# Kernel optimization log

Hardware: AMD Instinct MI355X
Metric: run time of the kernel (lower is better)

## Reference

```python
import jax, jax.numpy as jnp
import numpy as np

E, K, H, I, T = 32, 4, 1024, 1024, 1024
ALPHA, BETA = 1.702, 1.0  # swiglu_alpha, swiglu_beta from the module


def setup_inputs() -> dict:
    key = jax.random.key(0)
    k0, k1, k2, k3 = jax.random.split(key, 4)
    return {
        "hidden_states": jax.random.normal(k0, (T, H), jnp.float32),
        "gate_w": jax.random.normal(k1, (H, E), jnp.float32) * (H ** -0.5),
        "gate_b": jnp.zeros((E,), jnp.float32),
        # pair_wise_act=True: gate/up are interleaved along the last dim of w1's output
        "w1": jax.random.normal(k2, (E, H, 2 * I), jnp.float32) * (H ** -0.5),
        "b1": jnp.zeros((E, 2 * I), jnp.float32),
        "w2": jax.random.normal(k3, (E, I, H), jnp.float32) * (I ** -0.5),
        "b2": jnp.zeros((E, H), jnp.float32),
    }


def reference(hidden_states, gate_w, gate_b, w1, b1, w2, b2):
    # Router gate (ReplicatedLinear with bias)
    router_logits = hidden_states @ gate_w + gate_b            # [T, E]
    probs = jax.nn.softmax(router_logits, axis=-1)
    topk_w, topk_idx = jax.lax.top_k(probs, K)                 # [T, K]
    # renormalize (norm_topk_prob=True)
    topk_w = topk_w / jnp.sum(topk_w, axis=-1, keepdims=True)
    # combine weights per (expert, token): sum over slots where idx == e
    onehot = (topk_idx[None, :, :] == jnp.arange(E)[:, None, None])  # [E, T, K]
    combine_w = jnp.sum(onehot * topk_w[None, :, :], axis=-1)        # [E, T]
    # Expert MLPs (grouped GEMM expressed as dense-per-expert einsum)
    h = jnp.einsum('th,ehd->etd', hidden_states, w1) + b1[:, None, :]  # [E, T, 2I]
    gate = h[..., 0::2]   # interleaved pairwise gate
    up = h[..., 1::2]     # interleaved pairwise up
    act = (up + BETA) * gate * jax.nn.sigmoid(ALPHA * gate)           # [E, T, I]
    y = jnp.einsum('eti,eih->eth', act, w2) + b2[:, None, :]          # [E, T, H]
    # weighted combine across selected experts
    return jnp.einsum('eth,et->th', y, combine_w)                     # [T, H]
```

## Files before the change

kernel.cpp:

```cpp
#include <hip/hip_runtime.h>
#include <hip/hip_bf16.h>
#include <math.h>

#define E_ 32
#define K_ 4
#define H_ 1024
#define I_ 1024
#define T_ 1024
#define TWO_I 2048

typedef __attribute__((ext_vector_type(4))) float float4v;
typedef __attribute__((ext_vector_type(8))) short short8v;
typedef __attribute__((ext_vector_type(4))) short short4v;

__device__ __forceinline__ unsigned short f2bf(float f) {
    unsigned u = __float_as_uint(f);
    u = (u + 0x7FFFu + ((u >> 16) & 1u)) >> 16;
    return (unsigned short)u;
}
__device__ __forceinline__ short4v cvt4(float4v v) {
    union { unsigned u[2]; short4v s; } r;
    asm("v_cvt_pk_bf16_f32 %0, %1, %2" : "=v"(r.u[0]) : "v"(v[0]), "v"(v[1]));
    asm("v_cvt_pk_bf16_f32 %0, %1, %2" : "=v"(r.u[1]) : "v"(v[2]), "v"(v[3]));
    return r.s;
}
__device__ __forceinline__ int permpos(int k4) {
    return ((k4 >> 5) << 5) + (((k4 >> 2) & 3) << 3) + (((k4 >> 4) & 1) << 2);
}

__global__ __launch_bounds__(256) void zero_kernel(float* __restrict__ out,
                                                   int* __restrict__ counts) {
    int i = blockIdx.x * 256 + threadIdx.x;
    *(float4v*)(out + (size_t)i * 4) = (float4v){0.f, 0.f, 0.f, 0.f};
    if (blockIdx.x == 0 && threadIdx.x < E_) counts[threadIdx.x] = 0;
}

__global__ __launch_bounds__(256) void hs2bf_kernel(
    const float* __restrict__ hs, unsigned short* __restrict__ hsb) {
    int i = blockIdx.x * 256 + threadIdx.x;
    float4v v = *(const float4v*)(hs + (size_t)i * 4);
    *(short4v*)(hsb + (size_t)i * 4) = cvt4(v);
}

__global__ __launch_bounds__(256) void router_kernel(
    const float* __restrict__ hs, const float* __restrict__ gw,
    const float* __restrict__ gb, int* __restrict__ counts,
    int* __restrict__ token_list, float* __restrict__ weight_list) {
    int wv = threadIdx.x >> 6, lane = threadIdx.x & 63;
    int t = blockIdx.x * 4 + wv;
    int e = lane & 31;
    int half = lane >> 5;
    const float* hrow = hs + (size_t)t * H_;
    const float* gcol = gw + e;
    float a0 = 0.f, a1 = 0.f;
    int hb = half * 512;
#pragma unroll 4
    for (int h = 0; h < 512; h += 2) {
        a0 = fmaf(hrow[hb + h],     gcol[(size_t)(hb + h) * E_], a0);
        a1 = fmaf(hrow[hb + h + 1], gcol[(size_t)(hb + h + 1) * E_], a1);
    }
    float part = a0 + a1;
    part += __shfl_xor(part, 32);
    float cur = part + gb[e];

    int idx4[K_]; float val4[K_];
#pragma unroll
    for (int k = 0; k < K_; ++k) {
        float m = cur;
#pragma unroll
        for (int d = 1; d < 64; d <<= 1) m = fmaxf(m, __shfl_xor(m, d));
        unsigned long long b = __ballot(cur == m);
        int l = __ffsll(b) - 1;
        idx4[k] = l & 31; val4[k] = m;
        if (e == (l & 31)) cur = -INFINITY;
    }
    float mx = val4[0], s = 0.f, wv4[K_];
#pragma unroll
    for (int k = 0; k < K_; ++k) { wv4[k] = expf(val4[k] - mx); s += wv4[k]; }
    float inv = 1.f / s;
    if (lane < K_) {
        int ex = idx4[lane];
        int slot = atomicAdd(&counts[ex], 1);
        token_list[ex * T_ + slot] = t;
        weight_list[ex * T_ + slot] = wv4[lane] * inv;
    }
}

#define G_COMPUTE(BUF)                                                         \
    _Pragma("unroll")                                                          \
    for (int s = 0; s < 2; ++s) {                                              \
        short8v afr[4];                                                        \
        _Pragma("unroll")                                                      \
        for (int mi = 0; mi < 4; ++mi) {                                       \
            int row = wm * 64 + mi * 16 + l15;                                 \
            afr[mi] = *(const short8v*)&As[BUF][row * 64 + ((s * 32 + g * 8) ^ sw)]; \
        }                                                                      \
        short4v bl[2], bh[2];                                                  \
        _Pragma("unroll")                                                      \
        for (int ni = 0; ni < 2; ++ni) {                                       \
            unsigned ad = ((BUF) ? trb1 : trb0) + (unsigned)(ni * 2048 + s * 1024); \
            asm volatile("ds_read_b64_tr_b16 %0, %1" : "=v"(bl[ni]) : "v"(ad));     \
            asm volatile("ds_read_b64_tr_b16 %0, %1" : "=v"(bh[ni]) : "v"(ad + 512u)); \
        }                                                                      \
        asm volatile("s_waitcnt lgkmcnt(0)" ::: "memory");                     \
        __builtin_amdgcn_sched_barrier(0);                                     \
        _Pragma("unroll")                                                      \
        for (int ni = 0; ni < 2; ++ni) {                                       \
            short8v b;                                                         \
            b[0] = bl[ni][0]; b[1] = bl[ni][1]; b[2] = bl[ni][2]; b[3] = bl[ni][3]; \
            b[4] = bh[ni][0]; b[5] = bh[ni][1]; b[6] = bh[ni][2]; b[7] = bh[ni][3]; \
            _Pragma("unroll")                                                  \
            for (int mi = 0; mi < 4; ++mi)                                     \
                acc[mi][ni] = __builtin_amdgcn_mfma_f32_16x16x32_bf16(afr[mi], b, acc[mi][ni], 0, 0, 0); \
        }                                                                      \
    }

#define G_STEP(BUF, KN, BSTRIDE, ISLAST)                                       \
    {                                                                          \
        __syncthreads();                                                       \
        if (!(ISLAST)) {                                                       \
            _Pragma("unroll")                                                  \
            for (int i = 0; i < 4; ++i)                                        \
                ra[i] = aptr[i] ? *(const short8v*)(aptr[i] + (KN)) : z8;      \
            _Pragma("unroll")                                                  \
            for (int i = 0; i < 4; ++i)                                        \
                rb[i] = *(const float4v*)(bptrB + (size_t)(KN) * (BSTRIDE) + (size_t)(i * 16) * (BSTRIDE)); \
        }                                                                      \
        __builtin_amdgcn_sched_barrier(0);                                     \
        G_COMPUTE(BUF)                                                         \
        if (!(ISLAST)) {                                                       \
            _Pragma("unroll")                                                  \
            for (int i = 0; i < 4; ++i) {                                      \
                short8v v = ra[i];                                             \
                short4v lo, hi;                                                \
                lo[0] = v[0]; lo[1] = v[1]; lo[2] = v[2]; lo[3] = v[3];        \
                hi[0] = v[4]; hi[1] = v[5]; hi[2] = v[6]; hi[3] = v[7];        \
                *(short4v*)&As[(BUF) ^ 1][aw0[i]] = lo;                        \
                *(short4v*)&As[(BUF) ^ 1][aw1[i]] = hi;                        \
            }                                                                  \
            _Pragma("unroll")                                                  \
            for (int i = 0; i < 4; ++i) *(short4v*)&Bs[(BUF) ^ 1][bwidx[i]] = cvt4(rb[i]); \
        }                                                                      \
    }

__global__ __launch_bounds__(256, 3) void gemm1_kernel(
    const unsigned short* __restrict__ hsb, const float* __restrict__ w1,
    const float* __restrict__ b1, const int* __restrict__ counts,
    const int* __restrict__ token_list, unsigned short* __restrict__ actb) {
    int e = blockIdx.z;
    int cnt = counts[e];
    int m0 = blockIdx.y * 128;
    if (m0 >= cnt) return;
    int cb = blockIdx.x * 64;
    const float* w1e = w1 + (size_t)e * H_ * TWO_I;
    const int* tl = token_list + e * T_;

    __shared__ __align__(16) short As[2][128 * 64];
    __shared__ __align__(16) short Bs[2][64 * 64];

    int tid = threadIdx.x;
    int lane = tid & 63;
    int wid = tid >> 6;
    int wm = wid >> 1, wn = wid & 1;
    int g = lane >> 4;
    int l15 = lane & 15;
    int sw = (l15 & 7) << 3;
    unsigned trb0 = (unsigned)(size_t)(&Bs[0][0]) + (unsigned)(lane * 8) + (unsigned)(wn * 4096);
    unsigned trb1 = (unsigned)(size_t)(&Bs[1][0]) + (unsigned)(lane * 8) + (unsigned)(wn * 4096);

    int q = tid & 7;
    const unsigned short* aptr[4]; int aw0[4], aw1[4];
#pragma unroll
    for (int i = 0; i < 4; ++i) {
        int row = i * 32 + (tid >> 3);
        int gr = m0 + row;
        aptr[i] = (gr < cnt) ? hsb + (size_t)tl[gr] * H_ + q * 8 : nullptr;
        int swr = (row & 7) << 3;
        aw0[i] = row * 64 + (permpos(q * 8) ^ swr);
        aw1[i] = row * 64 + (permpos(q * 8 + 4) ^ swr);
    }
    int c4 = (tid & 15) << 2;
    const float* bptrB = w1e + (size_t)(tid >> 4) * TWO_I + cb + c4;
    int bwidx[4];
#pragma unroll
    for (int i = 0; i < 4; ++i) {
        int krow = i * 16 + (tid >> 4);
        bwidx[i] = ((c4 >> 4) * 16 + (krow >> 2)) * 64 + (krow & 3) * 16 + (c4 & 15);
    }

    float4v acc[4][2];
#pragma unroll
    for (int i = 0; i < 4; ++i)
#pragma unroll
        for (int j = 0; j < 2; ++j) acc[i][j] = (float4v){0.f, 0.f, 0.f, 0.f};

    short8v ra[4]; float4v rb[4];
    const short8v z8 = {0, 0, 0, 0, 0, 0, 0, 0};
#pragma unroll
    for (int i = 0; i < 4; ++i) ra[i] = aptr[i] ? *(const short8v*)(aptr[i]) : z8;
#pragma unroll
    for (int i = 0; i < 4; ++i) rb[i] = *(const float4v*)(bptrB + (size_t)(i * 16) * TWO_I);
#pragma unroll
    for (int i = 0; i < 4; ++i) {
        short8v v = ra[i];
        short4v lo, hi;
        lo[0] = v[0]; lo[1] = v[1]; lo[2] = v[2]; lo[3] = v[3];
        hi[0] = v[4]; hi[1] = v[5]; hi[2] = v[6]; hi[3] = v[7];
        *(short4v*)&As[0][aw0[i]] = lo;
        *(short4v*)&As[0][aw1[i]] = hi;
    }
#pragma unroll
    for (int i = 0; i < 4; ++i) *(short4v*)&Bs[0][bwidx[i]] = cvt4(rb[i]);

#pragma unroll 1
    for (int kk = 0; kk < H_; kk += 128) {
        G_STEP(0, kk + 64, TWO_I, false)
        G_STEP(1, kk + 128, TWO_I, (kk + 128) >= H_)
    }

    const float* b1e = b1 + (size_t)e * TWO_I;
#pragma unroll
    for (int mi = 0; mi < 4; ++mi) {
#pragma unroll
        for (int r = 0; r < 4; ++r) {
            int gm = m0 + wm * 64 + mi * 16 + g * 4 + r;
#pragma unroll
            for (int ni = 0; ni < 2; ++ni) {
                float v = acc[mi][ni][r];
                float o = __shfl_xor(v, 1);
                if (!(lane & 1) && gm < cnt) {
                    int wc = cb + wn * 32 + ni * 16 + l15;
                    float gate = v + b1e[wc];
                    float up   = o + b1e[wc + 1];
                    float sg = 1.f / (1.f + __expf(-1.702f * gate));
                    float av = (up + 1.f) * gate * sg;
                    actb[(size_t)(e * T_ + gm) * I_ + (wc >> 1)] = f2bf(av);
                }
            }
        }
    }
}

__global__ __launch_bounds__(256, 3) void gemm2_kernel(
    const unsigned short* __restrict__ actb, const float* __restrict__ w2,
    const float* __restrict__ b2, const int* __restrict__ counts,
    const int* __restrict__ token_list, const float* __restrict__ weight_list,
    float* __restrict__ out) {
    int e = blockIdx.z;
    int cnt = counts[e];
    int m0 = blockIdx.y * 128;
    if (m0 >= cnt) return;
    int h0 = (blockIdx.x >> 1) * 64;
    int kbase = (blockIdx.x & 1) * 512;
    const float* w2e = w2 + (size_t)e * I_ * H_;
    const int* tl = token_list + e * T_;

    __shared__ __align__(16) short As[2][128 * 64];
    __shared__ __align__(16) short Bs[2][64 * 64];

    int tid = threadIdx.x;
    int lane = tid & 63;
    int wid = tid >> 6;
    int wm = wid >> 1, wn = wid & 1;
    int g = lane >> 4;
    int l15 = lane & 15;
    int sw = (l15 & 7) << 3;
    unsigned trb0 = (unsigned)(size_t)(&Bs[0][0]) + (unsigned)(lane * 8) + (unsigned)(wn * 4096);
    unsigned trb1 = (unsigned)(size_t)(&Bs[1][0]) + (unsigned)(lane * 8) + (unsigned)(wn * 4096);

    int q = tid & 7;
    const unsigned short* aptr[4]; int aw0[4], aw1[4];
#pragma unroll
    for (int i = 0; i < 4; ++i) {
        int row = i * 32 + (tid >> 3);
        int gr = m0 + row;
        aptr[i] = (gr < cnt) ? actb + (size_t)(e * T_ + gr) * I_ + kbase + q * 8 : nullptr;
        int swr = (row & 7) << 3;
        aw0[i] = row * 64 + (permpos(q * 8) ^ swr);
        aw1[i] = row * 64 + (permpos(q * 8 + 4) ^ swr);
    }
    int c4 = (tid & 15) << 2;
    const float* bptrB = w2e + (size_t)(kbase + (tid >> 4)) * H_ + h0 + c4;
    int bwidx[4];
#pragma unroll
    for (int i = 0; i < 4; ++i) {
        int krow = i * 16 + (tid >> 4);
        bwidx[i] = ((c4 >> 4) * 16 + (krow >> 2)) * 64 + (krow & 3) * 16 + (c4 & 15);
    }

    float4v acc[4][2];
#pragma unroll
    for (int i = 0; i < 4; ++i)
#pragma unroll
        for (int j = 0; j < 2; ++j) acc[i][j] = (float4v){0.f, 0.f, 0.f, 0.f};

    short8v ra[4]; float4v rb[4];
    const short8v z8 = {0, 0, 0, 0, 0, 0, 0, 0};
#pragma unroll
    for (int i = 0; i < 4; ++i) ra[i] = aptr[i] ? *(const short8v*)(aptr[i]) : z8;
#pragma unroll
    for (int i = 0; i < 4; ++i) rb[i] = *(const float4v*)(bptrB + (size_t)(i * 16) * H_);
#pragma unroll
    for (int i = 0; i < 4; ++i) {
        short8v v = ra[i];
        short4v lo, hi;
        lo[0] = v[0]; lo[1] = v[1]; lo[2] = v[2]; lo[3] = v[3];
        hi[0] = v[4]; hi[1] = v[5]; hi[2] = v[6]; hi[3] = v[7];
        *(short4v*)&As[0][aw0[i]] = lo;
        *(short4v*)&As[0][aw1[i]] = hi;
    }
#pragma unroll
    for (int i = 0; i < 4; ++i) *(short4v*)&Bs[0][bwidx[i]] = cvt4(rb[i]);

#pragma unroll 1
    for (int kk = 0; kk < 512; kk += 128) {
        G_STEP(0, kk + 64, H_, false)
        G_STEP(1, kk + 128, H_, (kk + 128) >= 512)
    }

    const float* b2e = b2 + (size_t)e * H_;
    const float* wl = weight_list + e * T_;
    bool addbias = (kbase == 0);
#pragma unroll
    for (int mi = 0; mi < 4; ++mi) {
#pragma unroll
        for (int r = 0; r < 4; ++r) {
            int gm = m0 + wm * 64 + mi * 16 + g * 4 + r;
            if (gm < cnt) {
                int t = tl[gm];
                float wgt = wl[gm];
#pragma unroll
                for (int ni = 0; ni < 2; ++ni) {
                    int h = h0 + wn * 32 + ni * 16 + l15;
                    float v = acc[mi][ni][r];
                    if (addbias) v += b2e[h];
                    atomicAdd(&out[(size_t)t * H_ + h], v * wgt);
                }
            }
        }
    }
}

extern "C" void kernel_launch(void* const* d_in, const int* in_sizes, int n_in,
                              void* d_out, int out_size, void* d_ws, size_t ws_size,
                              hipStream_t stream) {
    const float* hs = (const float*)d_in[0];
    const float* gw = (const float*)d_in[1];
    const float* gb = (const float*)d_in[2];
    const float* w1 = (const float*)d_in[3];
    const float* b1 = (const float*)d_in[4];
    const float* w2 = (const float*)d_in[5];
    const float* b2 = (const float*)d_in[6];
    float* out = (float*)d_out;

    char* ws = (char*)d_ws;
    int*   counts      = (int*)ws;
    int*   token_list  = (int*)(ws + 4096);
    float* weight_list = (float*)(ws + 4096 + 131072);
    unsigned short* hsb  = (unsigned short*)(ws + (1 << 20));
    unsigned short* actb = (unsigned short*)(ws + (1 << 20) + (2 << 20));

    zero_kernel<<<(T_ * H_ / 4) / 256, 256, 0, stream>>>(out, counts);
    hs2bf_kernel<<<(T_ * H_ / 4) / 256, 256, 0, stream>>>(hs, hsb);
    router_kernel<<<T_ / 4, 256, 0, stream>>>(hs, gw, gb, counts, token_list, weight_list);
    gemm1_kernel<<<dim3(TWO_I / 64, T_ / 128, E_), 256, 0, stream>>>(
        hsb, w1, b1, counts, token_list, actb);
    gemm2_kernel<<<dim3((H_ / 64) * 2, T_ / 128, E_), 256, 0, stream>>>(
        actb, w2, b2, counts, token_list, weight_list, out);
}
```

Measured before the change: 201.6 us.

## Widen gemm1 N-tile to 128 and fuse zero/convert prep kernels

Result: slower. 217.6 us (+8.0%).

```diff
diff --git a/kernel.cpp b/kernel.cpp
--- a/kernel.cpp
+++ b/kernel.cpp
@@ -28,18 +28,14 @@
     return ((k4 >> 5) << 5) + (((k4 >> 2) & 3) << 3) + (((k4 >> 4) & 1) << 2);
 }
 
-__global__ __launch_bounds__(256) void zero_kernel(float* __restrict__ out,
-                                                   int* __restrict__ counts) {
-    int i = blockIdx.x * 256 + threadIdx.x;
-    *(float4v*)(out + (size_t)i * 4) = (float4v){0.f, 0.f, 0.f, 0.f};
-    if (blockIdx.x == 0 && threadIdx.x < E_) counts[threadIdx.x] = 0;
-}
-
-__global__ __launch_bounds__(256) void hs2bf_kernel(
-    const float* __restrict__ hs, unsigned short* __restrict__ hsb) {
+__global__ __launch_bounds__(256) void prep_kernel(
+    const float* __restrict__ hs, unsigned short* __restrict__ hsb,
+    float* __restrict__ out, int* __restrict__ counts) {
     int i = blockIdx.x * 256 + threadIdx.x;
     float4v v = *(const float4v*)(hs + (size_t)i * 4);
     *(short4v*)(hsb + (size_t)i * 4) = cvt4(v);
+    *(float4v*)(out + (size_t)i * 4) = (float4v){0.f, 0.f, 0.f, 0.f};
+    if (blockIdx.x == 0 && threadIdx.x < E_) counts[threadIdx.x] = 0;
 }
 
 __global__ __launch_bounds__(256) void router_kernel(
@@ -86,7 +82,7 @@
     }
 }
 
-#define G_COMPUTE(BUF)                                                         \
+#define G1_COMPUTE(BUF)                                                        \
     _Pragma("unroll")                                                          \
     for (int s = 0; s < 2; ++s) {                                              \
         short8v afr[4];                                                        \
@@ -95,9 +91,9 @@
             int row = wm * 64 + mi * 16 + l15;                                 \
             afr[mi] = *(const short8v*)&As[BUF][row * 64 + ((s * 32 + g * 8) ^ sw)]; \
         }                                                                      \
-        short4v bl[2], bh[2];                                                  \
-        _Pragma("unroll")                                                      \
-        for (int ni = 0; ni < 2; ++ni) {                                       \
+        short4v bl[4], bh[4];                                                  \
+        _Pragma("unroll")                                                      \
+        for (int ni = 0; ni < 4; ++ni) {                                       \
             unsigned ad = ((BUF) ? trb1 : trb0) + (unsigned)(ni * 2048 + s * 1024); \
             asm volatile("ds_read_b64_tr_b16 %0, %1" : "=v"(bl[ni]) : "v"(ad));     \
             asm volatile("ds_read_b64_tr_b16 %0, %1" : "=v"(bh[ni]) : "v"(ad + 512u)); \
@@ -105,7 +101,7 @@
         asm volatile("s_waitcnt lgkmcnt(0)" ::: "memory");                     \
         __builtin_amdgcn_sched_barrier(0);                                     \
         _Pragma("unroll")                                                      \
-        for (int ni = 0; ni < 2; ++ni) {                                       \
+        for (int ni = 0; ni < 4; ++ni) {                                       \
             short8v b;                                                         \
             b[0] = bl[ni][0]; b[1] = bl[ni][1]; b[2] = bl[ni][2]; b[3] = bl[ni][3]; \
             b[4] = bh[ni][0]; b[5] = bh[ni][1]; b[6] = bh[ni][2]; b[7] = bh[ni][3]; \
@@ -115,7 +111,7 @@
         }                                                                      \
     }
 
-#define G_STEP(BUF, KN, BSTRIDE, ISLAST)                                       \
+#define G1_STEP(BUF, KN, ISLAST)                                               \
     {                                                                          \
         __syncthreads();                                                       \
         if (!(ISLAST)) {                                                       \
@@ -123,11 +119,11 @@
             for (int i = 0; i < 4; ++i)                                        \
                 ra[i] = aptr[i] ? *(const short8v*)(aptr[i] + (KN)) : z8;      \
             _Pragma("unroll")                                                  \
-            for (int i = 0; i < 4; ++i)                                        \
-                rb[i] = *(const float4v*)(bptrB + (size_t)(KN) * (BSTRIDE) + (size_t)(i * 16) * (BSTRIDE)); \
+            for (int i = 0; i < 8; ++i)                                        \
+                rb[i] = *(const float4v*)(bptr[i] + (size_t)(KN) * TWO_I);     \
         }                                                                      \
         __builtin_amdgcn_sched_barrier(0);                                     \
-        G_COMPUTE(BUF)                                                         \
+        G1_COMPUTE(BUF)                                                        \
         if (!(ISLAST)) {                                                       \
             _Pragma("unroll")                                                  \
             for (int i = 0; i < 4; ++i) {                                      \
@@ -139,11 +135,11 @@
                 *(short4v*)&As[(BUF) ^ 1][aw1[i]] = hi;                        \
             }                                                                  \
             _Pragma("unroll")                                                  \
-            for (int i = 0; i < 4; ++i) *(short4v*)&Bs[(BUF) ^ 1][bwidx[i]] = cvt4(rb[i]); \
-        }                                                                      \
-    }
-
-__global__ __launch_bounds__(256, 3) void gemm1_kernel(
+            for (int i = 0; i < 8; ++i) *(short4v*)&Bs[(BUF) ^ 1][bwidx[i]] = cvt4(rb[i]); \
+        }                                                                      \
+    }
+
+__global__ __launch_bounds__(256, 2) void gemm1_kernel(
     const unsigned short* __restrict__ hsb, const float* __restrict__ w1,
     const float* __restrict__ b1, const int* __restrict__ counts,
     const int* __restrict__ token_list, unsigned short* __restrict__ actb) {
@@ -151,12 +147,12 @@
     int cnt = counts[e];
     int m0 = blockIdx.y * 128;
     if (m0 >= cnt) return;
-    int cb = blockIdx.x * 64;
+    int cb = blockIdx.x * 128;
     const float* w1e = w1 + (size_t)e * H_ * TWO_I;
     const int* tl = token_list + e * T_;
 
     __shared__ __align__(16) short As[2][128 * 64];
-    __shared__ __align__(16) short Bs[2][64 * 64];
+    __shared__ __align__(16) short Bs[2][8192];
 
     int tid = threadIdx.x;
     int lane = tid & 63;
@@ -165,8 +161,8 @@
     int g = lane >> 4;
     int l15 = lane & 15;
     int sw = (l15 & 7) << 3;
-    unsigned trb0 = (unsigned)(size_t)(&Bs[0][0]) + (unsigned)(lane * 8) + (unsigned)(wn * 4096);
-    unsigned trb1 = (unsigned)(size_t)(&Bs[1][0]) + (unsigned)(lane * 8) + (unsigned)(wn * 4096);
+    unsigned trb0 = (unsigned)(size_t)(&Bs[0][0]) + (unsigned)(lane * 8) + (unsigned)(wn * 8192);
+    unsigned trb1 = (unsigned)(size_t)(&Bs[1][0]) + (unsigned)(lane * 8) + (unsigned)(wn * 8192);
 
     int q = tid & 7;
     const unsigned short* aptr[4]; int aw0[4], aw1[4];
@@ -179,27 +175,28 @@
         aw0[i] = row * 64 + (permpos(q * 8) ^ swr);
         aw1[i] = row * 64 + (permpos(q * 8 + 4) ^ swr);
     }
-    int c4 = (tid & 15) << 2;
-    const float* bptrB = w1e + (size_t)(tid >> 4) * TWO_I + cb + c4;
-    int bwidx[4];
-#pragma unroll
-    for (int i = 0; i < 4; ++i) {
-        int krow = i * 16 + (tid >> 4);
-        bwidx[i] = ((c4 >> 4) * 16 + (krow >> 2)) * 64 + (krow & 3) * 16 + (c4 & 15);
-    }
-
-    float4v acc[4][2];
+    const float* bptr[8]; int bwidx[8];
+#pragma unroll
+    for (int i = 0; i < 8; ++i) {
+        int c = i * 256 + tid;
+        int krow = c >> 5;
+        int n4 = (c & 31) << 2;
+        bptr[i] = w1e + (size_t)krow * TWO_I + cb + n4;
+        bwidx[i] = ((n4 >> 4) * 16 + (krow >> 2)) * 64 + (krow & 3) * 16 + (n4 & 15);
+    }
+
+    float4v acc[4][4];
 #pragma unroll
     for (int i = 0; i < 4; ++i)
 #pragma unroll
-        for (int j = 0; j < 2; ++j) acc[i][j] = (float4v){0.f, 0.f, 0.f, 0.f};
-
-    short8v ra[4]; float4v rb[4];
+        for (int j = 0; j < 4; ++j) acc[i][j] = (float4v){0.f, 0.f, 0.f, 0.f};
+
+    short8v ra[4]; float4v rb[8];
     const short8v z8 = {0, 0, 0, 0, 0, 0, 0, 0};
 #pragma unroll
     for (int i = 0; i < 4; ++i) ra[i] = aptr[i] ? *(const short8v*)(aptr[i]) : z8;
 #pragma unroll
-    for (int i = 0; i < 4; ++i) rb[i] = *(const float4v*)(bptrB + (size_t)(i * 16) * TWO_I);
+    for (int i = 0; i < 8; ++i) rb[i] = *(const float4v*)(bptr[i]);
 #pragma unroll
     for (int i = 0; i < 4; ++i) {
         short8v v = ra[i];
@@ -210,12 +207,12 @@
         *(short4v*)&As[0][aw1[i]] = hi;
     }
 #pragma unroll
-    for (int i = 0; i < 4; ++i) *(short4v*)&Bs[0][bwidx[i]] = cvt4(rb[i]);
+    for (int i = 0; i < 8; ++i) *(short4v*)&Bs[0][bwidx[i]] = cvt4(rb[i]);
 
 #pragma unroll 1
     for (int kk = 0; kk < H_; kk += 128) {
-        G_STEP(0, kk + 64, TWO_I, false)
-        G_STEP(1, kk + 128, TWO_I, (kk + 128) >= H_)
+        G1_STEP(0, kk + 64, false)
+        G1_STEP(1, kk + 128, (kk + 128) >= H_)
     }
 
     const float* b1e = b1 + (size_t)e * TWO_I;
@@ -225,11 +222,11 @@
         for (int r = 0; r < 4; ++r) {
             int gm = m0 + wm * 64 + mi * 16 + g * 4 + r;
 #pragma unroll
-            for (int ni = 0; ni < 2; ++ni) {
+            for (int ni = 0; ni < 4; ++ni) {
                 float v = acc[mi][ni][r];
                 float o = __shfl_xor(v, 1);
                 if (!(lane & 1) && gm < cnt) {
-                    int wc = cb + wn * 32 + ni * 16 + l15;
+                    int wc = cb + wn * 64 + ni * 16 + l15;
                     float gate = v + b1e[wc];
                     float up   = o + b1e[wc + 1];
                     float sg = 1.f / (1.f + __expf(-1.702f * gate));
@@ -240,6 +237,63 @@
         }
     }
 }
+
+#define G2_COMPUTE(BUF)                                                        \
+    _Pragma("unroll")                                                          \
+    for (int s = 0; s < 2; ++s) {                                              \
+        short8v afr[4];                                                        \
+        _Pragma("unroll")                                                      \
+        for (int mi = 0; mi < 4; ++mi) {                                       \
+            int row = wm * 64 + mi * 16 + l15;                                 \
+            afr[mi] = *(const short8v*)&As[BUF][row * 64 + ((s * 32 + g * 8) ^ sw)]; \
+        }                                                                      \
+        short4v bl[2], bh[2];                                                  \
+        _Pragma("unroll")                                                      \
+        for (int ni = 0; ni < 2; ++ni) {                                       \
+            unsigned ad = ((BUF) ? trb1 : trb0) + (unsigned)(ni * 2048 + s * 1024); \
+            asm volatile("ds_read_b64_tr_b16 %0, %1" : "=v"(bl[ni]) : "v"(ad));     \
+            asm volatile("ds_read_b64_tr_b16 %0, %1" : "=v"(bh[ni]) : "v"(ad + 512u)); \
+        }                                                                      \
+        asm volatile("s_waitcnt lgkmcnt(0)" ::: "memory");                     \
+        __builtin_amdgcn_sched_barrier(0);                                     \
+        _Pragma("unroll")                                                      \
+        for (int ni = 0; ni < 2; ++ni) {                                       \
+            short8v b;                                                         \
+            b[0] = bl[ni][0]; b[1] = bl[ni][1]; b[2] = bl[ni][2]; b[3] = bl[ni][3]; \
+            b[4] = bh[ni][0]; b[5] = bh[ni][1]; b[6] = bh[ni][2]; b[7] = bh[ni][3]; \
+            _Pragma("unroll")                                                  \
+            for (int mi = 0; mi < 4; ++mi)                                     \
+                acc[mi][ni] = __builtin_amdgcn_mfma_f32_16x16x32_bf16(afr[mi], b, acc[mi][ni], 0, 0, 0); \
+        }                                                                      \
+    }
+
+#define G2_STEP(BUF, KN, ISLAST)                                               \
+    {                                                                          \
+        __syncthreads();                                                       \
+        if (!(ISLAST)) {                                                       \
+            _Pragma("unroll")                                                  \
+            for (int i = 0; i < 4; ++i)                                        \
+                ra[i] = aptr[i] ? *(const short8v*)(aptr[i] + (KN)) : z8;      \
+            _Pragma("unroll")                                                  \
+            for (int i = 0; i < 4; ++i)                                        \
+                rb[i] = *(const float4v*)(bptrB + (size_t)(KN) * H_ + (size_t)(i * 16) * H_); \
+        }                                                                      \
+        __builtin_amdgcn_sched_barrier(0);                                     \
+        G2_COMPUTE(BUF)                                                        \
+        if (!(ISLAST)) {                                                       \
+            _Pragma("unroll")                                                  \
+            for (int i = 0; i < 4; ++i) {                                      \
+                short8v v = ra[i];                                             \
+                short4v lo, hi;                                                \
+                lo[0] = v[0]; lo[1] = v[1]; lo[2] = v[2]; lo[3] = v[3];        \
+                hi[0] = v[4]; hi[1] = v[5]; hi[2] = v[6]; hi[3] = v[7];        \
+                *(short4v*)&As[(BUF) ^ 1][aw0[i]] = lo;                        \
+                *(short4v*)&As[(BUF) ^ 1][aw1[i]] = hi;                        \
+            }                                                                  \
+            _Pragma("unroll")                                                  \
+            for (int i = 0; i < 4; ++i) *(short4v*)&Bs[(BUF) ^ 1][bwidx[i]] = cvt4(rb[i]); \
+        }                                                                      \
+    }
 
 __global__ __launch_bounds__(256, 3) void gemm2_kernel(
     const unsigned short* __restrict__ actb, const float* __restrict__ w2,
@@ -314,8 +368,8 @@
 
 #pragma unroll 1
     for (int kk = 0; kk < 512; kk += 128) {
-        G_STEP(0, kk + 64, H_, false)
-        G_STEP(1, kk + 128, H_, (kk + 128) >= 512)
+        G2_STEP(0, kk + 64, false)
+        G2_STEP(1, kk + 128, (kk + 128) >= 512)
     }
 
     const float* b2e = b2 + (size_t)e * H_;
@@ -360,10 +414,9 @@
     unsigned short* hsb  = (unsigned short*)(ws + (1 << 20));
     unsigned short* actb = (unsigned short*)(ws + (1 << 20) + (2 << 20));
 
-    zero_kernel<<<(T_ * H_ / 4) / 256, 256, 0, stream>>>(out, counts);
-    hs2bf_kernel<<<(T_ * H_ / 4) / 256, 256, 0, stream>>>(hs, hsb);
+    prep_kernel<<<(T_ * H_ / 4) / 256, 256, 0, stream>>>(hs, hsb, out, counts);
     router_kernel<<<T_ / 4, 256, 0, stream>>>(hs, gw, gb, counts, token_list, weight_list);
-    gemm1_kernel<<<dim3(TWO_I / 64, T_ / 128, E_), 256, 0, stream>>>(
+    gemm1_kernel<<<dim3(TWO_I / 128, T_ / 128, E_), 256, 0, stream>>>(
         hsb, w1, b1, counts, token_list, actb);
     gemm2_kernel<<<dim3((H_ / 64) * 2, T_ / 128, E_), 256, 0, stream>>>(
         actb, w2, b2, counts, token_list, weight_list, out);
```
